# Optimization experiments

Hardware: AMD Instinct MI355X
Metric: run time of the kernel (lower is better)

Reference implementation:

```python
import jax, jax.numpy as jnp
import numpy as np

B, N, OBS, ACT, HID, GD, H = 1024, 64, 128, 16, 256, 64, 4
NEG_SLOPE = 0.2  # GAT leaky-relu alpha


def _gat(x, adj, W, a, concat):
    # x: (B,N,F), W: (H,F,D), a: (H,2D). Equivalent to concat([x_i,x_j]) . a
    # split as x_i.a1 + x_j.a2 -- same math, avoids the (B,H,N,N,2D) tensor.
    D = W.shape[-1]
    xt = jnp.einsum('bnf,hfd->bhnd', x, W)
    si = jnp.einsum('bhnd,hd->bhn', xt, a[:, :D])
    sj = jnp.einsum('bhnd,hd->bhn', xt, a[:, D:])
    s = jax.nn.leaky_relu(si[:, :, :, None] + sj[:, :, None, :], NEG_SLOPE)
    s = jnp.where(adj[:, None, :, :] == 0, -jnp.inf, s)
    w = jax.nn.softmax(s, axis=-1)
    out = jnp.einsum('bhij,bhjd->bhid', w, xt)
    if concat:
        b, n = x.shape[0], x.shape[1]
        return out.transpose(0, 2, 1, 3).reshape(b, n, -1)
    return out.mean(axis=1)


def _mlp3(x, w1, b1, w2, b2, w3, b3):
    # per-agent 3-layer MLP, weights stacked over agent axis n
    h = jax.nn.relu(jnp.einsum('bni,nih->bnh', x, w1) + b1)
    h = jax.nn.relu(jnp.einsum('bnh,nhk->bnk', h, w2) + b2)
    return jnp.einsum('bnk,nko->bno', h, w3) + b3


def _mlp2(x, w1, b1, w2, b2):
    h = jax.nn.relu(jnp.einsum('bni,nih->bnh', x, w1) + b1)
    return jnp.einsum('bnh,nho->bno', h, w2) + b2


def setup_inputs() -> dict:
    key = jax.random.key(0)
    ks = iter(jax.random.split(key, 64))

    def nrm(shape):
        fan_in = shape[-2] if len(shape) >= 2 else shape[-1]
        return jax.random.normal(next(ks), shape, jnp.float32) * np.float32(1.0 / np.sqrt(fan_in))

    AI = OBS + GD   # actor/critic input dim
    CI = OBS + ACT  # SCM / centralized per-agent input dim
    return dict(
        observations=jax.random.normal(next(ks), (B, N, OBS), jnp.float32),
        actions=jax.random.normal(next(ks), (B, N, ACT), jnp.float32),
        adj_matrix=jnp.ones((B, N, N), jnp.float32),
        causal_structure=jnp.eye(OBS, dtype=jnp.float32),
        gat_W=nrm((H, OBS, GD)), gat_a=nrm((H, 2 * GD)),
        cg_W0=nrm((H, OBS, GD)), cg_a0=nrm((H, 2 * GD)),
        cg_W1=nrm((H, H * GD, GD)), cg_a1=nrm((H, 2 * GD)),
        actor_w1=nrm((N, AI, HID)), actor_b1=jnp.zeros((N, HID), jnp.float32),
        actor_w2=nrm((N, HID, HID)), actor_b2=jnp.zeros((N, HID), jnp.float32),
        actor_w3=nrm((N, HID, ACT)), actor_b3=jnp.zeros((N, ACT), jnp.float32),
        critic_w1=nrm((N, AI, HID)), critic_b1=jnp.zeros((N, HID), jnp.float32),
        critic_w2=nrm((N, HID, HID)), critic_b2=jnp.zeros((N, HID), jnp.float32),
        critic_w3=nrm((N, HID, 1)), critic_b3=jnp.zeros((N, 1), jnp.float32),
        cent_w1=nrm((N * CI, HID)), cent_b1=jnp.zeros((HID,), jnp.float32),
        cent_w2=nrm((HID, HID)), cent_b2=jnp.zeros((HID,), jnp.float32),
        cent_w3=nrm((HID, N)), cent_b3=jnp.zeros((N,), jnp.float32),
        scm_causal=jnp.eye(N, dtype=jnp.float32),
        scm_mw1=nrm((N, CI, HID)), scm_mb1=jnp.zeros((N, HID), jnp.float32),
        scm_mw2=nrm((N, HID, HID)), scm_mb2=jnp.zeros((N, HID), jnp.float32),
        scm_mw3=nrm((N, HID, OBS)), scm_mb3=jnp.zeros((N, OBS), jnp.float32),
        scm_nw1=nrm((N, OBS, HID)), scm_nb1=jnp.zeros((N, HID), jnp.float32),
        scm_nw2=nrm((N, HID, OBS)), scm_nb2=jnp.zeros((N, OBS), jnp.float32),
    )


def reference(observations, actions, adj_matrix, causal_structure,
              gat_W, gat_a, cg_W0, cg_a0, cg_W1, cg_a1,
              actor_w1, actor_b1, actor_w2, actor_b2, actor_w3, actor_b3,
              critic_w1, critic_b1, critic_w2, critic_b2, critic_w3, critic_b3,
              cent_w1, cent_b1, cent_w2, cent_b2, cent_w3, cent_b3,
              scm_causal, scm_mw1, scm_mb1, scm_mw2, scm_mb2, scm_mw3, scm_mb3,
              scm_nw1, scm_nb1, scm_nw2, scm_nb2):
    # plain GAT communication features (concat=False -> head mean)
    gat_feat = _gat(observations, adj_matrix, gat_W, gat_a, False)
    # CausalGAT: causal mask on input features, then 2 GAT layers w/ ELU between
    xm = observations @ jax.nn.softmax(causal_structure, axis=-1)
    hcg = jax.nn.elu(_gat(xm, adj_matrix, cg_W0, cg_a0, True))
    causal_feat = _gat(hcg, adj_matrix, cg_W1, cg_a1, False)
    comm = gat_feat + causal_feat
    ai = jnp.concatenate([observations, comm], axis=-1)  # (B,N,OBS+GD)
    actor_out = _mlp3(ai, actor_w1, actor_b1, actor_w2, actor_b2, actor_w3, actor_b3)
    critic_out = _mlp3(ai, critic_w1, critic_b1, critic_w2, critic_b2, critic_w3, critic_b3)
    # centralized critic over flattened (obs, action) of all agents
    flat = jnp.concatenate([observations, actions], axis=-1).reshape(observations.shape[0], -1)
    hc = jax.nn.relu(flat @ cent_w1 + cent_b1)
    hc = jax.nn.relu(hc @ cent_w2 + cent_b2)
    cent_out = hc @ cent_w3 + cent_b3
    # SCM: per-agent causal mechanisms mixed by softmaxed causal matrix + noise model
    cw = jax.nn.softmax(scm_causal, axis=-1)
    combined = jnp.concatenate([observations, actions], axis=-1)
    ce = _mlp3(combined, scm_mw1, scm_mb1, scm_mw2, scm_mb2, scm_mw3, scm_mb3)
    se = jnp.einsum('ij,bjd->bid', cw, ce)
    noise = _mlp2(observations, scm_nw1, scm_nb1, scm_nw2, scm_nb2)
    scm_pred = se + noise
    return (actor_out, critic_out, cent_out, scm_pred)
```

## Files before the change

### kernel.cpp

```cpp
#include <hip/hip_runtime.h>
#include <hip/hip_bf16.h>
#include <math.h>

#define NB 1024
#define NAG 64
#define OBS 128
#define ACTD 16
#define HID 256
#define GD 64
#define NH 4

typedef short bhalf8 __attribute__((ext_vector_type(8)));
typedef float f32x4 __attribute__((ext_vector_type(4)));

__device__ inline unsigned short f2bf_u(float f) {
  __hip_bfloat16 h = __float2bfloat16(f);
  return *(unsigned short*)&h;
}
__device__ inline float bfu2f(unsigned short u) {
  unsigned v = ((unsigned)u) << 16;
  return *(float*)&v;
}
__device__ inline unsigned pk2(float x, float y) {
  float2 f2; f2.x = x; f2.y = y;
  __hip_bfloat162 h = __float22bfloat162_rn(f2);
  return *(unsigned*)&h;
}
__device__ inline unsigned fbits(float x) { return *(unsigned*)&x; }
__device__ inline float bcast(unsigned u) { return *(float*)&u; }
__device__ inline unsigned pkhi(float x, float y) {
  return (fbits(x) >> 16) | (fbits(y) & 0xFFFF0000u);
}
__device__ inline float hif(float x) {
  return bcast(fbits(x) & 0xFFFF0000u);
}

__global__ __launch_bounds__(64) void softmax_rows_k(const float* __restrict__ in,
                                                     float* __restrict__ out, int n) {
  int row = blockIdx.x;
  int lane = threadIdx.x;
  const float* r = in + (size_t)row * n;
  float m = -INFINITY;
  for (int j = lane; j < n; j += 64) m = fmaxf(m, r[j]);
#pragma unroll
  for (int off = 32; off; off >>= 1) m = fmaxf(m, __shfl_xor(m, off));
  float s = 0.f;
  for (int j = lane; j < n; j += 64) s += expf(r[j] - m);
#pragma unroll
  for (int off = 32; off; off >>= 1) s += __shfl_xor(s, off);
  float inv = 1.f / s;
  for (int j = lane; j < n; j += 64) out[(size_t)row * n + j] = expf(r[j] - m) * inv;
}

__global__ void cwbf_k(const float* __restrict__ cwsm, unsigned short* __restrict__ cw1,
                       unsigned short* __restrict__ cw2) {
  int idx = blockIdx.x * 256 + threadIdx.x;
  if (idx >= 4096) return;
  float v = cwsm[idx];
  unsigned short hi = f2bf_u(v);
  cw1[idx] = hi;
  cw2[idx] = f2bf_u(v - bfu2f(hi));
}

__global__ __launch_bounds__(256) void transpose_cvt_k(const float* __restrict__ in,
                                                       unsigned short* __restrict__ out,
                                                       int K, int N) {
  __shared__ float t[32][33];
  int k0 = blockIdx.x * 32, n0 = blockIdx.y * 32, z = blockIdx.z;
  int tx = threadIdx.x, ty = threadIdx.y;
  const float* ib = in + (size_t)z * K * N;
  unsigned short* ob = out + (size_t)z * N * K;
#pragma unroll
  for (int i = 0; i < 4; ++i) {
    int k = k0 + ty + 8 * i, n = n0 + tx;
    if (k < K && n < N) t[ty + 8 * i][tx] = ib[(size_t)k * N + n];
  }
  __syncthreads();
#pragma unroll
  for (int i = 0; i < 4; ++i) {
    int n = n0 + ty + 8 * i, k = k0 + tx;
    if (n < N && k < K) ob[(size_t)n * K + k] = f2bf_u(t[tx][ty + 8 * i]);
  }
}

__global__ void repack_wT_k(const float* __restrict__ W, unsigned short* __restrict__ WcT, int F) {
  int idx = blockIdx.x * 256 + threadIdx.x;
  if (idx >= NH * F * 64) return;
  int d = idx & 63;
  int f = (idx >> 6) % F;
  int h = idx / (F * 64);
  WcT[((size_t)(h * 64 + d)) * F + f] = f2bf_u(W[idx]);
}

__global__ __launch_bounds__(256) void gemm_mfma_k(
    const float* __restrict__ A, const unsigned short* __restrict__ BT,
    const float* __restrict__ bias, float* __restrict__ C,
    int M, int N, int K,
    long long lda, long long ldc,
    long long aBS, long long btBS, long long biasBS, long long cBS,
    int act, int kPerSplit) {
  __shared__ unsigned short As[2][64 * 40];
  __shared__ unsigned short Bs[2][64 * 40];
  int tid = threadIdx.x;
  int wave = tid >> 6, lane = tid & 63;
  int m0 = blockIdx.x * 64, n0 = blockIdx.y * 64;
  int z = blockIdx.z;
  const float* Ab;
  const unsigned short* Bb;
  const float* biasb = nullptr;
  float* Cb;
  int k_begin, k_end;
  if (kPerSplit > 0) {
    Ab = A; Bb = BT; Cb = C + (long long)z * cBS;
    k_begin = z * kPerSplit;
    k_end = k_begin + kPerSplit;
    if (k_end > K) k_end = K;
  } else {
    Ab = A + (long long)z * aBS;
    Bb = BT + (long long)z * btBS;
    if (bias) biasb = bias + (long long)z * biasBS;
    Cb = C + (long long)z * cBS;
    k_begin = 0; k_end = K;
  }
  int sr = tid >> 2;
  int sk = (tid & 3) * 8;
  int fr = lane & 15;
  int kq = (lane >> 4) * 8;

  f32x4 zf = {0.f, 0.f, 0.f, 0.f};
  f32x4 acc[4] = {zf, zf, zf, zf};

  const unsigned short* bRow = Bb + (long long)(n0 + sr) * K;
  bool bValid = (n0 + sr) < N;
  const float* aRow = Ab + (long long)(m0 + sr) * lda;

  int nt = (k_end - k_begin + 31) / 32;

  float av[8];
  uint4 bv;

  auto LOADT = [&](int t) {
    int kk = k_begin + 32 * t + sk;
    if (kk + 7 < k_end) {
      const float* ap = aRow + kk;
      *(float4*)&av[0] = *(const float4*)ap;
      *(float4*)&av[4] = *(const float4*)(ap + 4);
    } else {
#pragma unroll
      for (int j = 0; j < 8; ++j) av[j] = (kk + j < k_end) ? aRow[kk + j] : 0.f;
    }
    bv.x = bv.y = bv.z = bv.w = 0u;
    if (bValid) {
      if (kk + 7 < k_end) {
        bv = *(const uint4*)(bRow + kk);
      } else {
        unsigned short tb[8];
#pragma unroll
        for (int j = 0; j < 8; ++j) tb[j] = (kk + j < k_end) ? bRow[kk + j] : (unsigned short)0;
        bv.x = (unsigned)tb[0] | ((unsigned)tb[1] << 16);
        bv.y = (unsigned)tb[2] | ((unsigned)tb[3] << 16);
        bv.z = (unsigned)tb[4] | ((unsigned)tb[5] << 16);
        bv.w = (unsigned)tb[6] | ((unsigned)tb[7] << 16);
      }
    }
  };
  auto STORE = [&](int buf) {
    uint4 aw;
    aw.x = pk2(av[0], av[1]); aw.y = pk2(av[2], av[3]);
    aw.z = pk2(av[4], av[5]); aw.w = pk2(av[6], av[7]);
    *(uint4*)&As[buf][sr * 40 + sk] = aw;
    *(uint4*)&Bs[buf][sr * 40 + sk] = bv;
  };

  LOADT(0);
  STORE(0);
  if (nt > 1) LOADT(1);
  __syncthreads();

  for (int t = 0; t < nt; ++t) {
    int cur = t & 1;
    if (t + 1 < nt) {
      STORE(cur ^ 1);
      if (t + 2 < nt) LOADT(t + 2);
    }
    bhalf8 af = *(bhalf8*)&As[cur][(16 * wave + fr) * 40 + kq];
#pragma unroll
    for (int t4 = 0; t4 < 4; ++t4) {
      bhalf8 bf = *(bhalf8*)&Bs[cur][(16 * t4 + fr) * 40 + kq];
      acc[t4] = __builtin_amdgcn_mfma_f32_16x16x32_bf16(af, bf, acc[t4], 0, 0, 0);
    }
    if (t + 1 < nt) __syncthreads();
  }
  int rb = (lane >> 4) * 4;
#pragma unroll
  for (int t = 0; t < 4; ++t) {
    int col = n0 + 16 * t + fr;
    if (col < N) {
      float bv2 = biasb ? biasb[col] : 0.f;
#pragma unroll
      for (int r = 0; r < 4; ++r) {
        long long row = m0 + 16 * wave + rb + r;
        float v = acc[t][r] + bv2;
        if (act == 1) v = fmaxf(v, 0.f);
        Cb[row * ldc + col] = v;
      }
    }
  }
}

__global__ __launch_bounds__(256, 4) void gemm_mfma128_k(
    const float* __restrict__ A, const unsigned short* __restrict__ BT,
    const float* __restrict__ bias, float* __restrict__ C,
    int M, int N, int K,
    long long lda, long long ldc,
    long long aBS, long long btBS, long long biasBS, long long cBS,
    int act, int kPerSplit) {
  __shared__ unsigned short As[2][128 * 40];
  __shared__ unsigned short Bs[2][128 * 40];
  int tid = threadIdx.x;
  int wave = tid >> 6, lane = tid & 63;
  int m0 = blockIdx.x * 128, n0 = blockIdx.y * 128;
  int z = blockIdx.z;
  const float* Ab;
  const unsigned short* Bb;
  const float* biasb = nullptr;
  float* Cb;
  int k_begin, k_end;
  if (kPerSplit > 0) {
    Ab = A; Bb = BT; Cb = C + (long long)z * cBS;
    k_begin = z * kPerSplit;
    k_end = k_begin + kPerSplit;
    if (k_end > K) k_end = K;
  } else {
    Ab = A + (long long)z * aBS;
    Bb = BT + (long long)z * btBS;
    if (bias) biasb = bias + (long long)z * biasBS;
    Cb = C + (long long)z * cBS;
    k_begin = 0; k_end = K;
  }
  int sr = tid >> 1;
  int sk = (tid & 1) * 16;
  int mq = (wave >> 1) * 64;
  int nq = (wave & 1) * 64;
  int fr = lane & 15;
  int kq = (lane >> 4) * 8;

  f32x4 zf = {0.f, 0.f, 0.f, 0.f};
  f32x4 acc[4][4];
#pragma unroll
  for (int i = 0; i < 4; ++i)
#pragma unroll
    for (int j = 0; j < 4; ++j) acc[i][j] = zf;

  const float* aRow = Ab + (long long)(m0 + sr) * lda;
  const unsigned short* bRow = Bb + (long long)(n0 + sr) * K;
  bool bValid = (n0 + sr) < N;

  int nt = (k_end - k_begin + 31) / 32;

  float av[16];
  uint4 bv0, bv1;

  auto LOADT = [&](int t) {
    int kk = k_begin + 32 * t + sk;
    if (kk + 15 < k_end) {
      const float* ap = aRow + kk;
      *(float4*)&av[0]  = *(const float4*)ap;
      *(float4*)&av[4]  = *(const float4*)(ap + 4);
      *(float4*)&av[8]  = *(const float4*)(ap + 8);
      *(float4*)&av[12] = *(const float4*)(ap + 12);
    } else {
#pragma unroll
      for (int j = 0; j < 16; ++j) av[j] = (kk + j < k_end) ? aRow[kk + j] : 0.f;
    }
    bv0.x = bv0.y = bv0.z = bv0.w = 0u;
    bv1.x = bv1.y = bv1.z = bv1.w = 0u;
    if (bValid) {
      if (kk + 15 < k_end) {
        bv0 = *(const uint4*)(bRow + kk);
        bv1 = *(const uint4*)(bRow + kk + 8);
      } else {
        unsigned short tb[16];
#pragma unroll
        for (int j = 0; j < 16; ++j) tb[j] = (kk + j < k_end) ? bRow[kk + j] : (unsigned short)0;
        bv0.x = (unsigned)tb[0] | ((unsigned)tb[1] << 16);
        bv0.y = (unsigned)tb[2] | ((unsigned)tb[3] << 16);
        bv0.z = (unsigned)tb[4] | ((unsigned)tb[5] << 16);
        bv0.w = (unsigned)tb[6] | ((unsigned)tb[7] << 16);
        bv1.x = (unsigned)tb[8] | ((unsigned)tb[9] << 16);
        bv1.y = (unsigned)tb[10] | ((unsigned)tb[11] << 16);
        bv1.z = (unsigned)tb[12] | ((unsigned)tb[13] << 16);
        bv1.w = (unsigned)tb[14] | ((unsigned)tb[15] << 16);
      }
    }
  };
  auto STORE = [&](int buf) {
    uint4 aw0, aw1;
    aw0.x = pk2(av[0], av[1]);   aw0.y = pk2(av[2], av[3]);
    aw0.z = pk2(av[4], av[5]);   aw0.w = pk2(av[6], av[7]);
    aw1.x = pk2(av[8], av[9]);   aw1.y = pk2(av[10], av[11]);
    aw1.z = pk2(av[12], av[13]); aw1.w = pk2(av[14], av[15]);
    *(uint4*)&As[buf][sr * 40 + sk] = aw0;
    *(uint4*)&As[buf][sr * 40 + sk + 8] = aw1;
    *(uint4*)&Bs[buf][sr * 40 + sk] = bv0;
    *(uint4*)&Bs[buf][sr * 40 + sk + 8] = bv1;
  };

  LOADT(0);
  STORE(0);
  if (nt > 1) LOADT(1);
  __syncthreads();

  for (int t = 0; t < nt; ++t) {
    int cur = t & 1;
    if (t + 1 < nt) {
      STORE(cur ^ 1);
      if (t + 2 < nt) LOADT(t + 2);
    }
    bhalf8 af[4], bf[4];
#pragma unroll
    for (int i = 0; i < 4; ++i) af[i] = *(bhalf8*)&As[cur][(mq + 16 * i + fr) * 40 + kq];
#pragma unroll
    for (int j = 0; j < 4; ++j) bf[j] = *(bhalf8*)&Bs[cur][(nq + 16 * j + fr) * 40 + kq];
#pragma unroll
    for (int i = 0; i < 4; ++i)
#pragma unroll
      for (int j = 0; j < 4; ++j)
        acc[i][j] = __builtin_amdgcn_mfma_f32_16x16x32_bf16(af[i], bf[j], acc[i][j], 0, 0, 0);
    if (t + 1 < nt) __syncthreads();
  }
  int rb = (lane >> 4) * 4;
#pragma unroll
  for (int j = 0; j < 4; ++j) {
    int col = n0 + nq + 16 * j + fr;
    if (col < N) {
      float bv2 = biasb ? biasb[col] : 0.f;
#pragma unroll
      for (int i = 0; i < 4; ++i) {
#pragma unroll
        for (int r = 0; r < 4; ++r) {
          long long row = m0 + mq + 16 * i + rb + r;
          float v = acc[i][j][r] + bv2;
          if (act == 1) v = fmaxf(v, 0.f);
          Cb[row * ldc + col] = v;
        }
      }
    }
  }
}

__global__ __launch_bounds__(256, 4) void gat_attn4_k(
    const float* __restrict__ xt, const float* __restrict__ a,
    const float* __restrict__ adj, float* __restrict__ out, int mode) {
  int b = blockIdx.x;
  int tid = threadIdx.x;
  int wave = tid >> 6, lane = tid & 63;
  __shared__ unsigned short xT1[64 * 72];
  __shared__ unsigned short xT2[64 * 72];
  __shared__ unsigned short P1[64 * 72];
  __shared__ unsigned short P2[64 * 72];
  __shared__ float si_s[64], sj_s[64];

  const float* adjb = adj + (size_t)b * 4096;
  float adjv[16];
#pragma unroll
  for (int r = 0; r < 16; ++r) adjv[r] = adjb[(size_t)(wave * 16 + r) * 64 + lane];

  int lrow = tid >> 2;
  int cg = tid & 3;
  int fr = lane & 15;
  int kq = (lane >> 4) * 8;
  int ibase = wave * 16;

  bhalf8 ones;
#pragma unroll
  for (int u = 0; u < 8; ++u) ones[u] = (short)0x3F80;

  f32x4 zf = {0.f, 0.f, 0.f, 0.f};
  f32x4 accm[4] = {zf, zf, zf, zf};

  for (int h = 0; h < 4; ++h) {
    const float* xcol = xt + ((size_t)(b * 64 + 16 * wave)) * 256 + h * 64 + lane;
    float v[16];
#pragma unroll
    for (int u = 0; u < 16; ++u) v[u] = xcol[(size_t)u * 256];

    const float* xrow = xt + ((size_t)(b * 64 + lrow)) * 256 + h * 64 + cg * 16;
    const float* ah = a + h * 128;
    float p1 = 0.f, p2 = 0.f;
#pragma unroll
    for (int q = 0; q < 4; ++q) {
      float4 rv = *(const float4*)(xrow + 4 * q);
      int c = cg * 16 + 4 * q;
      p1 += rv.x * ah[c] + rv.y * ah[c + 1] + rv.z * ah[c + 2] + rv.w * ah[c + 3];
      p2 += rv.x * ah[64 + c] + rv.y * ah[64 + c + 1] + rv.z * ah[64 + c + 2] + rv.w * ah[64 + c + 3];
    }
    p1 += __shfl_xor(p1, 1); p1 += __shfl_xor(p1, 2);
    p2 += __shfl_xor(p2, 1); p2 += __shfl_xor(p2, 2);
    if (cg == 0) { si_s[lrow] = p1; sj_s[lrow] = p2; }

    {
      float lo[16];
      uint4 h0, h1, l0, l1;
#pragma unroll
      for (int u = 0; u < 16; ++u) lo[u] = v[u] - hif(v[u]);
      h0.x = pkhi(v[0], v[1]);    h0.y = pkhi(v[2], v[3]);
      h0.z = pkhi(v[4], v[5]);    h0.w = pkhi(v[6], v[7]);
      h1.x = pkhi(v[8], v[9]);    h1.y = pkhi(v[10], v[11]);
      h1.z = pkhi(v[12], v[13]);  h1.w = pkhi(v[14], v[15]);
      l0.x = pkhi(lo[0], lo[1]);   l0.y = pkhi(lo[2], lo[3]);
      l0.z = pkhi(lo[4], lo[5]);   l0.w = pkhi(lo[6], lo[7]);
      l1.x = pkhi(lo[8], lo[9]);   l1.y = pkhi(lo[10], lo[11]);
      l1.z = pkhi(lo[12], lo[13]); l1.w = pkhi(lo[14], lo[15]);
      int base = lane * 72 + 16 * wave;
      *(uint4*)&xT1[base] = h0;
      *(uint4*)&xT1[base + 8] = h1;
      *(uint4*)&xT2[base] = l0;
      *(uint4*)&xT2[base + 8] = l1;
    }
    __syncthreads();

    float sjv = sj_s[lane];
    float maxsj = sjv;
#pragma unroll
    for (int off = 32; off; off >>= 1) maxsj = fmaxf(maxsj, __shfl_xor(maxsj, off));
#pragma unroll
    for (int r = 0; r < 16; ++r) {
      int i = ibase + r;
      float siv = si_s[i];
      float tM = siv + maxsj;
      float Mi = tM > 0.f ? tM : 0.2f * tM;
      float e = siv + sjv;
      e = e > 0.f ? e : 0.2f * e;
      float p = (adjv[r] == 0.f) ? 0.f : __expf(e - Mi);
      unsigned up = fbits(p);
      float phf = bcast(up & 0xFFFF0000u);
      P1[i * 72 + lane] = (unsigned short)(up >> 16);
      float plo = p - phf;
      P2[i * 72 + lane] = (unsigned short)(fbits(plo) >> 16);
    }

    bhalf8 a1[2], a2[2];
#pragma unroll
    for (int ks = 0; ks < 2; ++ks) {
      a1[ks] = *(bhalf8*)&P1[(ibase + fr) * 72 + ks * 32 + kq];
      a2[ks] = *(bhalf8*)&P2[(ibase + fr) * 72 + ks * 32 + kq];
    }
    f32x4 accS = zf;
#pragma unroll
    for (int ks = 0; ks < 2; ++ks) {
      accS = __builtin_amdgcn_mfma_f32_16x16x32_bf16(a1[ks], ones, accS, 0, 0, 0);
      accS = __builtin_amdgcn_mfma_f32_16x16x32_bf16(a2[ks], ones, accS, 0, 0, 0);
    }
    f32x4 acc[4] = {zf, zf, zf, zf};
#pragma unroll
    for (int ks = 0; ks < 2; ++ks) {
#pragma unroll
      for (int t = 0; t < 4; ++t) {
        bhalf8 b1 = *(bhalf8*)&xT1[(16 * t + fr) * 72 + ks * 32 + kq];
        bhalf8 b2 = *(bhalf8*)&xT2[(16 * t + fr) * 72 + ks * 32 + kq];
        acc[t] = __builtin_amdgcn_mfma_f32_16x16x32_bf16(a1[ks], b1, acc[t], 0, 0, 0);
        acc[t] = __builtin_amdgcn_mfma_f32_16x16x32_bf16(a1[ks], b2, acc[t], 0, 0, 0);
        acc[t] = __builtin_amdgcn_mfma_f32_16x16x32_bf16(a2[ks], b1, acc[t], 0, 0, 0);
      }
    }
    f32x4 inv;
#pragma unroll
    for (int r = 0; r < 4; ++r) inv[r] = (accS[r] > 0.f) ? 1.f / accS[r] : 0.f;

    int rb = (lane >> 4) * 4;
    if (mode == 2) {
#pragma unroll
      for (int t = 0; t < 4; ++t) {
#pragma unroll
        for (int r = 0; r < 4; ++r) {
          int i = ibase + rb + r;
          float vv = acc[t][r] * inv[r];
          vv = vv > 0.f ? vv : __expf(vv) - 1.f;
          out[((size_t)(b * 64 + i)) * 256 + h * 64 + 16 * t + fr] = vv;
        }
      }
    } else {
#pragma unroll
      for (int t = 0; t < 4; ++t)
#pragma unroll
        for (int r = 0; r < 4; ++r) accm[t][r] += 0.25f * acc[t][r] * inv[r];
    }
    __syncthreads();
  }

  if (mode != 2) {
    int rb = (lane >> 4) * 4;
    float* cb = out + (size_t)b * 4096;
#pragma unroll
    for (int t = 0; t < 4; ++t) {
#pragma unroll
      for (int r = 0; r < 4; ++r) {
        int i = ibase + rb + r;
        int col = 16 * t + fr;
        if (mode == 1) cb[i * 64 + col] += accm[t][r];
        else cb[i * 64 + col] = accm[t][r];
      }
    }
  }
}

__global__ void build_ai_k(const float* __restrict__ obs, const float* __restrict__ comm,
                           float* __restrict__ ai) {
  size_t idx = (size_t)blockIdx.x * 256 + threadIdx.x;
  if (idx >= (size_t)NB * NAG * 192) return;
  int c = (int)(idx % 192);
  size_t bn = idx / 192;
  ai[idx] = (c < 128) ? obs[bn * 128 + c] : comm[bn * 64 + (c - 128)];
}

__global__ void build_combined_k(const float* __restrict__ obs, const float* __restrict__ act,
                                 float* __restrict__ cmb) {
  size_t idx = (size_t)blockIdx.x * 256 + threadIdx.x;
  if (idx >= (size_t)NB * NAG * 144) return;
  int c = (int)(idx % 144);
  size_t bn = idx / 144;
  cmb[idx] = (c < 128) ? obs[bn * 128 + c] : act[bn * 16 + (c - 128)];
}

__global__ void reduce_bias_relu_k(const float* __restrict__ part, const float* __restrict__ bias,
                                   float* __restrict__ out) {
  int idx = blockIdx.x * 256 + threadIdx.x;
  float s = 0.f;
#pragma unroll
  for (int zz = 0; zz < 16; ++zz) s += part[(size_t)zz * 262144 + idx];
  s += bias[idx & 255];
  out[idx] = fmaxf(s, 0.f);
}

__global__ __launch_bounds__(256, 4) void se_noise_mfma_k(
    const unsigned short* __restrict__ cw1, const unsigned short* __restrict__ cw2,
    const float* __restrict__ ce, const float* __restrict__ nz,
    float* __restrict__ out) {
  int b = blockIdx.x;
  int tid = threadIdx.x;
  int wave = tid >> 6, lane = tid & 63;
  __shared__ unsigned short xT1[128 * 72];
  __shared__ unsigned short xT2[128 * 72];

  int dd = tid & 127;
  int jh = tid >> 7;
  const float* cecol = ce + (size_t)b * 8192 + dd;
#pragma unroll
  for (int c = 0; c < 2; ++c) {
    int j0 = jh * 32 + c * 16;
    float v[16], lo[16];
#pragma unroll
    for (int u = 0; u < 16; ++u) v[u] = cecol[(size_t)(j0 + u) * 128];
#pragma unroll
    for (int u = 0; u < 16; ++u) lo[u] = v[u] - hif(v[u]);
    uint4 h0, h1, l0, l1;
    h0.x = pkhi(v[0], v[1]);    h0.y = pkhi(v[2], v[3]);
    h0.z = pkhi(v[4], v[5]);    h0.w = pkhi(v[6], v[7]);
    h1.x = pkhi(v[8], v[9]);    h1.y = pkhi(v[10], v[11]);
    h1.z = pkhi(v[12], v[13]);  h1.w = pkhi(v[14], v[15]);
    l0.x = pkhi(lo[0], lo[1]);   l0.y = pkhi(lo[2], lo[3]);
    l0.z = pkhi(lo[4], lo[5]);   l0.w = pkhi(lo[6], lo[7]);
    l1.x = pkhi(lo[8], lo[9]);   l1.y = pkhi(lo[10], lo[11]);
    l1.z = pkhi(lo[12], lo[13]); l1.w = pkhi(lo[14], lo[15]);
    int base = dd * 72 + j0;
    *(uint4*)&xT1[base] = h0;
    *(uint4*)&xT1[base + 8] = h1;
    *(uint4*)&xT2[base] = l0;
    *(uint4*)&xT2[base + 8] = l1;
  }
  __syncthreads();

  int fr = lane & 15;
  int kq = (lane >> 4) * 8;
  int dq = wave * 32;

  bhalf8 bb1[2][2], bb2[2][2];
#pragma unroll
  for (int dt = 0; dt < 2; ++dt)
#pragma unroll
    for (int ks = 0; ks < 2; ++ks) {
      bb1[dt][ks] = *(bhalf8*)&xT1[(dq + dt * 16 + fr) * 72 + ks * 32 + kq];
      bb2[dt][ks] = *(bhalf8*)&xT2[(dq + dt * 16 + fr) * 72 + ks * 32 + kq];
    }

  f32x4 zf = {0.f, 0.f, 0.f, 0.f};
  f32x4 acc[4][2];
#pragma unroll
  for (int it = 0; it < 4; ++it)
#pragma unroll
    for (int dt = 0; dt < 2; ++dt) acc[it][dt] = zf;

#pragma unroll
  for (int it = 0; it < 4; ++it) {
    bhalf8 a1[2], a2[2];
#pragma unroll
    for (int ks = 0; ks < 2; ++ks) {
      a1[ks] = *(const bhalf8*)(cw1 + (it * 16 + fr) * 64 + ks * 32 + kq);
      a2[ks] = *(const bhalf8*)(cw2 + (it * 16 + fr) * 64 + ks * 32 + kq);
    }
#pragma unroll
    for (int dt = 0; dt < 2; ++dt)
#pragma unroll
      for (int ks = 0; ks < 2; ++ks) {
        acc[it][dt] = __builtin_amdgcn_mfma_f32_16x16x32_bf16(a1[ks], bb1[dt][ks], acc[it][dt], 0, 0, 0);
        acc[it][dt] = __builtin_amdgcn_mfma_f32_16x16x32_bf16(a1[ks], bb2[dt][ks], acc[it][dt], 0, 0, 0);
        acc[it][dt] = __builtin_amdgcn_mfma_f32_16x16x32_bf16(a2[ks], bb1[dt][ks], acc[it][dt], 0, 0, 0);
      }
  }

  int rb = (lane >> 4) * 4;
#pragma unroll
  for (int it = 0; it < 4; ++it)
#pragma unroll
    for (int dt = 0; dt < 2; ++dt) {
      int dcol = dq + dt * 16 + fr;
#pragma unroll
      for (int r = 0; r < 4; ++r) {
        int i = it * 16 + rb + r;
        size_t off = (size_t)b * 8192 + (size_t)i * 128 + dcol;
        out[off] = acc[it][dt][r] + nz[off];
      }
    }
}

extern "C" void kernel_launch(void* const* d_in, const int* in_sizes, int n_in,
                              void* d_out, int out_size, void* d_ws, size_t ws_size,
                              hipStream_t stream) {
  (void)in_sizes; (void)n_in; (void)out_size; (void)ws_size;
  const float* obs = (const float*)d_in[0];
  const float* acts = (const float*)d_in[1];
  const float* adj = (const float*)d_in[2];
  const float* causal = (const float*)d_in[3];
  const float* gat_W = (const float*)d_in[4];
  const float* gat_a = (const float*)d_in[5];
  const float* cg_W0 = (const float*)d_in[6];
  const float* cg_a0 = (const float*)d_in[7];
  const float* cg_W1 = (const float*)d_in[8];
  const float* cg_a1 = (const float*)d_in[9];
  const float* aw1 = (const float*)d_in[10]; const float* ab1 = (const float*)d_in[11];
  const float* aw2 = (const float*)d_in[12]; const float* ab2 = (const float*)d_in[13];
  const float* aw3 = (const float*)d_in[14]; const float* ab3 = (const float*)d_in[15];
  const float* crw1 = (const float*)d_in[16]; const float* crb1 = (const float*)d_in[17];
  const float* crw2 = (const float*)d_in[18]; const float* crb2 = (const float*)d_in[19];
  const float* crw3 = (const float*)d_in[20]; const float* crb3 = (const float*)d_in[21];
  const float* cew1 = (const float*)d_in[22]; const float* ceb1 = (const float*)d_in[23];
  const float* cew2 = (const float*)d_in[24]; const float* ceb2 = (const float*)d_in[25];
  const float* cew3 = (const float*)d_in[26]; const float* ceb3 = (const float*)d_in[27];
  const float* scm_causal = (const float*)d_in[28];
  const float* mw1 = (const float*)d_in[29]; const float* mb1 = (const float*)d_in[30];
  const float* mw2 = (const float*)d_in[31]; const float* mb2 = (const float*)d_in[32];
  const float* mw3 = (const float*)d_in[33]; const float* mb3 = (const float*)d_in[34];
  const float* nw1 = (const float*)d_in[35]; const float* nb1 = (const float*)d_in[36];
  const float* nw2 = (const float*)d_in[37]; const float* nb2 = (const float*)d_in[38];

  float* ws = (float*)d_ws;
  float* Ssm  = ws;
  float* cwsm = ws + 16384;
  float* comm = ws + 20480;
  float* AI   = ws + 4214784;
  float* H1   = ws + 16797696;
  float* HCG  = ws + 33574912;
  unsigned short* wbf = (unsigned short*)(ws + 50352128);
  unsigned short* SsmT  = wbf;
  unsigned short* wcT   = wbf + 16384;
  unsigned short* aw1T  = wbf + 81920;
  unsigned short* aw2T  = wbf + 3227648;
  unsigned short* aw3T  = wbf + 7421952;
  unsigned short* crw1T = wbf + 7684096;
  unsigned short* crw2T = wbf + 10829824;
  unsigned short* crw3T = wbf + 15024128;
  unsigned short* cew1T = wbf + 15040512;
  unsigned short* cew2T = wbf + 17399808;
  unsigned short* cew3T = wbf + 17465344;
  unsigned short* mw1T  = wbf + 17481728;
  unsigned short* mw2T  = wbf + 19841024;
  unsigned short* mw3T  = wbf + 24035328;
  unsigned short* nw1T  = wbf + 26132480;
  unsigned short* nw2T  = wbf + 28229632;
  unsigned short* cw1g = (unsigned short*)ws;
  unsigned short* cw2g = cw1g + 4096;

  float* out_actor = (float*)d_out;
  float* out_critic = out_actor + 1048576;
  float* out_cent = out_critic + 65536;
  float* out_scm = out_cent + 65536;

  auto GEMM64 = [&](const float* A, const unsigned short* BT, const float* bias, float* C,
                    int M, int N, int K, long long lda, long long ldc,
                    long long aBS, long long btBS, long long biasBS, long long cBS,
                    int act, int gz, int kPerSplit) {
    dim3 grid(M / 64, (N + 63) / 64, gz);
    hipLaunchKernelGGL(gemm_mfma_k, grid, dim3(256), 0, stream, A, BT, bias, C, M, N, K,
                       lda, ldc, aBS, btBS, biasBS, cBS, act, kPerSplit);
  };
  auto GEMM128 = [&](const float* A, const unsigned short* BT, const float* bias, float* C,
                     int M, int N, int K, long long lda, long long ldc,
                     long long aBS, long long btBS, long long biasBS, long long cBS,
                     int act, int gz, int kPerSplit) {
    dim3 grid(M / 128, (N + 127) / 128, gz);
    hipLaunchKernelGGL(gemm_mfma128_k, grid, dim3(256), 0, stream, A, BT, bias, C, M, N, K,
                       lda, ldc, aBS, btBS, biasBS, cBS, act, kPerSplit);
  };
  auto TRN = [&](const float* in, unsigned short* out, int Z, int K, int N) {
    dim3 grid((K + 31) / 32, (N + 31) / 32, Z);
    hipLaunchKernelGGL(transpose_cvt_k, grid, dim3(32, 8), 0, stream, in, out, K, N);
  };

  hipLaunchKernelGGL(softmax_rows_k, dim3(128), dim3(64), 0, stream, causal, Ssm, 128);
  hipLaunchKernelGGL(softmax_rows_k, dim3(64), dim3(64), 0, stream, scm_causal, cwsm, 64);
  TRN(Ssm, SsmT, 1, 128, 128);
  hipLaunchKernelGGL(cwbf_k, dim3(16), dim3(256), 0, stream, cwsm, cw1g, cw2g);
  TRN(aw1, aw1T, 64, 192, 256);  TRN(aw2, aw2T, 64, 256, 256);  TRN(aw3, aw3T, 64, 256, 16);
  TRN(crw1, crw1T, 64, 192, 256); TRN(crw2, crw2T, 64, 256, 256); TRN(crw3, crw3T, 64, 256, 1);
  TRN(cew1, cew1T, 1, 9216, 256); TRN(cew2, cew2T, 1, 256, 256);  TRN(cew3, cew3T, 1, 256, 64);
  TRN(mw1, mw1T, 64, 144, 256);  TRN(mw2, mw2T, 64, 256, 256);  TRN(mw3, mw3T, 64, 256, 128);
  TRN(nw1, nw1T, 64, 128, 256);  TRN(nw2, nw2T, 64, 256, 128);

  hipLaunchKernelGGL(repack_wT_k, dim3((NH * 128 * 64 + 255) / 256), dim3(256), 0, stream, gat_W, wcT, 128);
  GEMM128(obs, wcT, nullptr, H1, 65536, 256, 128, 128, 256, 0, 0, 0, 0, 0, 1, 0);
  hipLaunchKernelGGL(gat_attn4_k, dim3(1024), dim3(256), 0, stream, H1, gat_a, adj, comm, 0);

  GEMM128(obs, SsmT, nullptr, HCG, 65536, 128, 128, 128, 128, 0, 0, 0, 0, 0, 1, 0);
  hipLaunchKernelGGL(repack_wT_k, dim3((NH * 128 * 64 + 255) / 256), dim3(256), 0, stream, cg_W0, wcT, 128);
  GEMM128(HCG, wcT, nullptr, H1, 65536, 256, 128, 128, 256, 0, 0, 0, 0, 0, 1, 0);
  hipLaunchKernelGGL(gat_attn4_k, dim3(1024), dim3(256), 0, stream, H1, cg_a0, adj, HCG, 2);
  hipLaunchKernelGGL(repack_wT_k, dim3((NH * 256 * 64 + 255) / 256), dim3(256), 0, stream, cg_W1, wcT, 256);
  GEMM128(HCG, wcT, nullptr, H1, 65536, 256, 256, 256, 256, 0, 0, 0, 0, 0, 1, 0);
  hipLaunchKernelGGL(gat_attn4_k, dim3(1024), dim3(256), 0, stream, H1, cg_a1, adj, comm, 1);

  hipLaunchKernelGGL(build_ai_k, dim3((12582912 + 255) / 256), dim3(256), 0, stream, obs, comm, AI);

  GEMM128(AI, aw1T, ab1, H1, 1024, 256, 192, 12288, 16384, 192, 49152, 256, 256, 1, 64, 0);
  GEMM128(H1, aw2T, ab2, HCG, 1024, 256, 256, 16384, 16384, 256, 65536, 256, 256, 1, 64, 0);
  GEMM64(HCG, aw3T, ab3, out_actor, 1024, 16, 256, 16384, 1024, 256, 4096, 16, 16, 0, 64, 0);

  GEMM128(AI, crw1T, crb1, H1, 1024, 256, 192, 12288, 16384, 192, 49152, 256, 256, 1, 64, 0);
  GEMM128(H1, crw2T, crb2, HCG, 1024, 256, 256, 16384, 16384, 256, 65536, 256, 256, 1, 64, 0);
  GEMM64(HCG, crw3T, crb3, out_critic, 1024, 1, 256, 16384, 64, 256, 256, 1, 1, 0, 64, 0);

  hipLaunchKernelGGL(build_combined_k, dim3((9437184 + 255) / 256), dim3(256), 0, stream, obs, acts, AI);
  GEMM128(AI, cew1T, nullptr, H1, 1024, 256, 9216, 9216, 256, 0, 0, 0, 262144, 0, 16, 576);
  hipLaunchKernelGGL(reduce_bias_relu_k, dim3(1024), dim3(256), 0, stream, H1, ceb1, HCG);
  GEMM64(HCG, cew2T, ceb2, H1, 1024, 256, 256, 256, 256, 0, 0, 0, 0, 1, 1, 0);
  GEMM64(H1, cew3T, ceb3, out_cent, 1024, 64, 256, 256, 64, 0, 0, 0, 0, 0, 1, 0);

  GEMM128(AI, mw1T, mb1, H1, 1024, 256, 144, 9216, 16384, 144, 36864, 256, 256, 1, 64, 0);
  GEMM128(H1, mw2T, mb2, HCG, 1024, 256, 256, 16384, 16384, 256, 65536, 256, 256, 1, 64, 0);
  GEMM128(HCG, mw3T, mb3, AI, 1024, 128, 256, 16384, 8192, 256, 32768, 128, 128, 0, 64, 0);

  GEMM128(obs, nw1T, nb1, H1, 1024, 256, 128, 8192, 16384, 128, 32768, 256, 256, 1, 64, 0);
  GEMM128(H1, nw2T, nb2, HCG, 1024, 128, 256, 16384, 8192, 256, 32768, 128, 128, 0, 64, 0);

  hipLaunchKernelGGL(se_noise_mfma_k, dim3(1024), dim3(256), 0, stream, cw1g, cw2g, AI, HCG, out_scm);
}
```

Before: 929.2 us.

## Store intermediate activations in bf16 between GEMMs to halve memory traffic

```diff
diff --git a/kernel.cpp b/kernel.cpp
--- a/kernel.cpp
+++ b/kernel.cpp
@@ -93,33 +93,32 @@
 }
 
 __global__ __launch_bounds__(256) void gemm_mfma_k(
-    const float* __restrict__ A, const unsigned short* __restrict__ BT,
-    const float* __restrict__ bias, float* __restrict__ C,
+    const void* __restrict__ A, const unsigned short* __restrict__ BT,
+    const float* __restrict__ bias, void* __restrict__ C,
     int M, int N, int K,
     long long lda, long long ldc,
     long long aBS, long long btBS, long long biasBS, long long cBS,
-    int act, int kPerSplit) {
+    int act, int kPerSplit, int aBf, int cBf) {
   __shared__ unsigned short As[2][64 * 40];
   __shared__ unsigned short Bs[2][64 * 40];
   int tid = threadIdx.x;
   int wave = tid >> 6, lane = tid & 63;
   int m0 = blockIdx.x * 64, n0 = blockIdx.y * 64;
   int z = blockIdx.z;
-  const float* Ab;
+  long long aOff, cOff;
   const unsigned short* Bb;
   const float* biasb = nullptr;
-  float* Cb;
   int k_begin, k_end;
   if (kPerSplit > 0) {
-    Ab = A; Bb = BT; Cb = C + (long long)z * cBS;
+    aOff = 0; Bb = BT; cOff = (long long)z * cBS;
     k_begin = z * kPerSplit;
     k_end = k_begin + kPerSplit;
     if (k_end > K) k_end = K;
   } else {
-    Ab = A + (long long)z * aBS;
+    aOff = (long long)z * aBS;
     Bb = BT + (long long)z * btBS;
     if (bias) biasb = bias + (long long)z * biasBS;
-    Cb = C + (long long)z * cBS;
+    cOff = (long long)z * cBS;
     k_begin = 0; k_end = K;
   }
   int sr = tid >> 2;
@@ -132,22 +131,40 @@
 
   const unsigned short* bRow = Bb + (long long)(n0 + sr) * K;
   bool bValid = (n0 + sr) < N;
-  const float* aRow = Ab + (long long)(m0 + sr) * lda;
+  const float* aRowF = (const float*)A + aOff + (long long)(m0 + sr) * lda;
+  const unsigned short* aRowH = (const unsigned short*)A + aOff + (long long)(m0 + sr) * lda;
+  float* CbF = (float*)C + cOff;
+  unsigned short* CbH = (unsigned short*)C + cOff;
 
   int nt = (k_end - k_begin + 31) / 32;
 
   float av[8];
+  uint4 awh;
   uint4 bv;
 
   auto LOADT = [&](int t) {
     int kk = k_begin + 32 * t + sk;
-    if (kk + 7 < k_end) {
-      const float* ap = aRow + kk;
-      *(float4*)&av[0] = *(const float4*)ap;
-      *(float4*)&av[4] = *(const float4*)(ap + 4);
+    if (aBf) {
+      if (kk + 7 < k_end) {
+        awh = *(const uint4*)(aRowH + kk);
+      } else {
+        unsigned short ta[8];
+#pragma unroll
+        for (int j = 0; j < 8; ++j) ta[j] = (kk + j < k_end) ? aRowH[kk + j] : (unsigned short)0;
+        awh.x = (unsigned)ta[0] | ((unsigned)ta[1] << 16);
+        awh.y = (unsigned)ta[2] | ((unsigned)ta[3] << 16);
+        awh.z = (unsigned)ta[4] | ((unsigned)ta[5] << 16);
+        awh.w = (unsigned)ta[6] | ((unsigned)ta[7] << 16);
+      }
     } else {
-#pragma unroll
-      for (int j = 0; j < 8; ++j) av[j] = (kk + j < k_end) ? aRow[kk + j] : 0.f;
+      if (kk + 7 < k_end) {
+        const float* ap = aRowF + kk;
+        *(float4*)&av[0] = *(const float4*)ap;
+        *(float4*)&av[4] = *(const float4*)(ap + 4);
+      } else {
+#pragma unroll
+        for (int j = 0; j < 8; ++j) av[j] = (kk + j < k_end) ? aRowF[kk + j] : 0.f;
+      }
     }
     bv.x = bv.y = bv.z = bv.w = 0u;
     if (bValid) {
@@ -166,8 +183,12 @@
   };
   auto STORE = [&](int buf) {
     uint4 aw;
-    aw.x = pk2(av[0], av[1]); aw.y = pk2(av[2], av[3]);
-    aw.z = pk2(av[4], av[5]); aw.w = pk2(av[6], av[7]);
+    if (aBf) {
+      aw = awh;
+    } else {
+      aw.x = pk2(av[0], av[1]); aw.y = pk2(av[2], av[3]);
+      aw.z = pk2(av[4], av[5]); aw.w = pk2(av[6], av[7]);
+    }
     *(uint4*)&As[buf][sr * 40 + sk] = aw;
     *(uint4*)&Bs[buf][sr * 40 + sk] = bv;
   };
@@ -202,40 +223,40 @@
         long long row = m0 + 16 * wave + rb + r;
         float v = acc[t][r] + bv2;
         if (act == 1) v = fmaxf(v, 0.f);
-        Cb[row * ldc + col] = v;
+        if (cBf) CbH[row * ldc + col] = f2bf_u(v);
+        else CbF[row * ldc + col] = v;
       }
     }
   }
 }
 
 __global__ __launch_bounds__(256, 4) void gemm_mfma128_k(
-    const float* __restrict__ A, const unsigned short* __restrict__ BT,
-    const float* __restrict__ bias, float* __restrict__ C,
+    const void* __restrict__ A, const unsigned short* __restrict__ BT,
+    const float* __restrict__ bias, void* __restrict__ C,
     int M, int N, int K,
     long long lda, long long ldc,
     long long aBS, long long btBS, long long biasBS, long long cBS,
-    int act, int kPerSplit) {
+    int act, int kPerSplit, int aBf, int cBf) {
   __shared__ unsigned short As[2][128 * 40];
   __shared__ unsigned short Bs[2][128 * 40];
   int tid = threadIdx.x;
   int wave = tid >> 6, lane = tid & 63;
   int m0 = blockIdx.x * 128, n0 = blockIdx.y * 128;
   int z = blockIdx.z;
-  const float* Ab;
+  long long aOff, cOff;
   const unsigned short* Bb;
   const float* biasb = nullptr;
-  float* Cb;
   int k_begin, k_end;
   if (kPerSplit > 0) {
-    Ab = A; Bb = BT; Cb = C + (long long)z * cBS;
+    aOff = 0; Bb = BT; cOff = (long long)z * cBS;
     k_begin = z * kPerSplit;
     k_end = k_begin + kPerSplit;
     if (k_end > K) k_end = K;
   } else {
-    Ab = A + (long long)z * aBS;
+    aOff = (long long)z * aBS;
     Bb = BT + (long long)z * btBS;
     if (bias) biasb = bias + (long long)z * biasBS;
-    Cb = C + (long long)z * cBS;
+    cOff = (long long)z * cBS;
     k_begin = 0; k_end = K;
   }
   int sr = tid >> 1;
@@ -252,26 +273,49 @@
 #pragma unroll
     for (int j = 0; j < 4; ++j) acc[i][j] = zf;
 
-  const float* aRow = Ab + (long long)(m0 + sr) * lda;
+  const float* aRowF = (const float*)A + aOff + (long long)(m0 + sr) * lda;
+  const unsigned short* aRowH = (const unsigned short*)A + aOff + (long long)(m0 + sr) * lda;
   const unsigned short* bRow = Bb + (long long)(n0 + sr) * K;
   bool bValid = (n0 + sr) < N;
+  float* CbF = (float*)C + cOff;
+  unsigned short* CbH = (unsigned short*)C + cOff;
 
   int nt = (k_end - k_begin + 31) / 32;
 
   float av[16];
+  uint4 awh0, awh1;
   uint4 bv0, bv1;
 
   auto LOADT = [&](int t) {
     int kk = k_begin + 32 * t + sk;
-    if (kk + 15 < k_end) {
-      const float* ap = aRow + kk;
-      *(float4*)&av[0]  = *(const float4*)ap;
-      *(float4*)&av[4]  = *(const float4*)(ap + 4);
-      *(float4*)&av[8]  = *(const float4*)(ap + 8);
-      *(float4*)&av[12] = *(const float4*)(ap + 12);
+    if (aBf) {
+      if (kk + 15 < k_end) {
+        awh0 = *(const uint4*)(aRowH + kk);
+        awh1 = *(const uint4*)(aRowH + kk + 8);
+      } else {
+        unsigned short ta[16];
+#pragma unroll
+        for (int j = 0; j < 16; ++j) ta[j] = (kk + j < k_end) ? aRowH[kk + j] : (unsigned short)0;
+        awh0.x = (unsigned)ta[0] | ((unsigned)ta[1] << 16);
+        awh0.y = (unsigned)ta[2] | ((unsigned)ta[3] << 16);
+        awh0.z = (unsigned)ta[4] | ((unsigned)ta[5] << 16);
+        awh0.w = (unsigned)ta[6] | ((unsigned)ta[7] << 16);
+        awh1.x = (unsigned)ta[8] | ((unsigned)ta[9] << 16);
+        awh1.y = (unsigned)ta[10] | ((unsigned)ta[11] << 16);
+        awh1.z = (unsigned)ta[12] | ((unsigned)ta[13] << 16);
+        awh1.w = (unsigned)ta[14] | ((unsigned)ta[15] << 16);
+      }
     } else {
-#pragma unroll
-      for (int j = 0; j < 16; ++j) av[j] = (kk + j < k_end) ? aRow[kk + j] : 0.f;
+      if (kk + 15 < k_end) {
+        const float* ap = aRowF + kk;
+        *(float4*)&av[0]  = *(const float4*)ap;
+        *(float4*)&av[4]  = *(const float4*)(ap + 4);
+        *(float4*)&av[8]  = *(const float4*)(ap + 8);
+        *(float4*)&av[12] = *(const float4*)(ap + 12);
+      } else {
+#pragma unroll
+        for (int j = 0; j < 16; ++j) av[j] = (kk + j < k_end) ? aRowF[kk + j] : 0.f;
+      }
     }
     bv0.x = bv0.y = bv0.z = bv0.w = 0u;
     bv1.x = bv1.y = bv1.z = bv1.w = 0u;
@@ -296,10 +340,14 @@
   };
   auto STORE = [&](int buf) {
     uint4 aw0, aw1;
-    aw0.x = pk2(av[0], av[1]);   aw0.y = pk2(av[2], av[3]);
-    aw0.z = pk2(av[4], av[5]);   aw0.w = pk2(av[6], av[7]);
-    aw1.x = pk2(av[8], av[9]);   aw1.y = pk2(av[10], av[11]);
-    aw1.z = pk2(av[12], av[13]); aw1.w = pk2(av[14], av[15]);
+    if (aBf) {
+      aw0 = awh0; aw1 = awh1;
+    } else {
+      aw0.x = pk2(av[0], av[1]);   aw0.y = pk2(av[2], av[3]);
+      aw0.z = pk2(av[4], av[5]);   aw0.w = pk2(av[6], av[7]);
+      aw1.x = pk2(av[8], av[9]);   aw1.y = pk2(av[10], av[11]);
+      aw1.z = pk2(av[12], av[13]); aw1.w = pk2(av[14], av[15]);
+    }
     *(uint4*)&As[buf][sr * 40 + sk] = aw0;
     *(uint4*)&As[buf][sr * 40 + sk + 8] = aw1;
     *(uint4*)&Bs[buf][sr * 40 + sk] = bv0;
@@ -342,7 +390,8 @@
           long long row = m0 + mq + 16 * i + rb + r;
           float v = acc[i][j][r] + bv2;
           if (act == 1) v = fmaxf(v, 0.f);
-          Cb[row * ldc + col] = v;
+          if (cBf) CbH[row * ldc + col] = f2bf_u(v);
+          else CbF[row * ldc + col] = v;
         }
       }
     }
@@ -470,6 +519,7 @@
 
     int rb = (lane >> 4) * 4;
     if (mode == 2) {
+      unsigned short* outh = (unsigned short*)out;
 #pragma unroll
       for (int t = 0; t < 4; ++t) {
 #pragma unroll
@@ -477,7 +527,7 @@
           int i = ibase + rb + r;
           float vv = acc[t][r] * inv[r];
           vv = vv > 0.f ? vv : __expf(vv) - 1.f;
-          out[((size_t)(b * 64 + i)) * 256 + h * 64 + 16 * t + fr] = vv;
+          outh[((size_t)(b * 64 + i)) * 256 + h * 64 + 16 * t + fr] = f2bf_u(vv);
         }
       }
     } else {
@@ -506,31 +556,33 @@
 }
 
 __global__ void build_ai_k(const float* __restrict__ obs, const float* __restrict__ comm,
-                           float* __restrict__ ai) {
+                           unsigned short* __restrict__ ai) {
   size_t idx = (size_t)blockIdx.x * 256 + threadIdx.x;
   if (idx >= (size_t)NB * NAG * 192) return;
   int c = (int)(idx % 192);
   size_t bn = idx / 192;
-  ai[idx] = (c < 128) ? obs[bn * 128 + c] : comm[bn * 64 + (c - 128)];
+  float v = (c < 128) ? obs[bn * 128 + c] : comm[bn * 64 + (c - 128)];
+  ai[idx] = f2bf_u(v);
 }
 
 __global__ void build_combined_k(const float* __restrict__ obs, const float* __restrict__ act,
-                                 float* __restrict__ cmb) {
+                                 unsigned short* __restrict__ cmb) {
   size_t idx = (size_t)blockIdx.x * 256 + threadIdx.x;
   if (idx >= (size_t)NB * NAG * 144) return;
   int c = (int)(idx % 144);
   size_t bn = idx / 144;
-  cmb[idx] = (c < 128) ? obs[bn * 128 + c] : act[bn * 16 + (c - 128)];
+  float v = (c < 128) ? obs[bn * 128 + c] : act[bn * 16 + (c - 128)];
+  cmb[idx] = f2bf_u(v);
 }
 
 __global__ void reduce_bias_relu_k(const float* __restrict__ part, const float* __restrict__ bias,
-                                   float* __restrict__ out) {
+                                   unsigned short* __restrict__ out) {
   int idx = blockIdx.x * 256 + threadIdx.x;
   float s = 0.f;
 #pragma unroll
   for (int zz = 0; zz < 16; ++zz) s += part[(size_t)zz * 262144 + idx];
   s += bias[idx & 255];
-  out[idx] = fmaxf(s, 0.f);
+  out[idx] = f2bf_u(fmaxf(s, 0.f));
 }
 
 __global__ __launch_bounds__(256, 4) void se_noise_mfma_k(
@@ -680,27 +732,30 @@
   unsigned short* nw2T  = wbf + 28229632;
   unsigned short* cw1g = (unsigned short*)ws;
   unsigned short* cw2g = cw1g + 4096;
+  unsigned short* AIb  = (unsigned short*)AI;
+  unsigned short* H1b  = (unsigned short*)H1;
+  unsigned short* HCGb = (unsigned short*)HCG;
 
   float* out_actor = (float*)d_out;
   float* out_critic = out_actor + 1048576;
   float* out_cent = out_critic + 65536;
   float* out_scm = out_cent + 65536;
 
-  auto GEMM64 = [&](const float* A, const unsigned short* BT, const float* bias, float* C,
+  auto GEMM64 = [&](const void* A, const unsigned short* BT, const float* bias, void* C,
                     int M, int N, int K, long long lda, long long ldc,
                     long long aBS, long long btBS, long long biasBS, long long cBS,
-                    int act, int gz, int kPerSplit) {
+                    int act, int gz, int kPerSplit, int aBf, int cBf) {
     dim3 grid(M / 64, (N + 63) / 64, gz);
     hipLaunchKernelGGL(gemm_mfma_k, grid, dim3(256), 0, stream, A, BT, bias, C, M, N, K,
-                       lda, ldc, aBS, btBS, biasBS, cBS, act, kPerSplit);
+                       lda, ldc, aBS, btBS, biasBS, cBS, act, kPerSplit, aBf, cBf);
   };
-  auto GEMM128 = [&](const float* A, const unsigned short* BT, const float* bias, float* C,
+  auto GEMM128 = [&](const void* A, const unsigned short* BT, const float* bias, void* C,
                      int M, int N, int K, long long lda, long long ldc,
                      long long aBS, long long btBS, long long biasBS, long long cBS,
-                     int act, int gz, int kPerSplit) {
+                     int act, int gz, int kPerSplit, int aBf, int cBf) {
     dim3 grid(M / 128, (N + 127) / 128, gz);
     hipLaunchKernelGGL(gemm_mfma128_k, grid, dim3(256), 0, stream, A, BT, bias, C, M, N, K,
-                       lda, ldc, aBS, btBS, biasBS, cBS, act, kPerSplit);
+                       lda, ldc, aBS, btBS, biasBS, cBS, act, kPerSplit, aBf, cBf);
   };
   auto TRN = [&](const float* in, unsigned short* out, int Z, int K, int N) {
     dim3 grid((K + 31) / 32, (N + 31) / 32, Z);
@@ -718,39 +773,39 @@
   TRN(nw1, nw1T, 64, 128, 256);  TRN(nw2, nw2T, 64, 256, 128);
 
   hipLaunchKernelGGL(repack_wT_k, dim3((NH * 128 * 64 + 255) / 256), dim3(256), 0, stream, gat_W, wcT, 128);
-  GEMM128(obs, wcT, nullptr, H1, 65536, 256, 128, 128, 256, 0, 0, 0, 0, 0, 1, 0);
+  GEMM128(obs, wcT, nullptr, H1, 65536, 256, 128, 128, 256, 0, 0, 0, 0, 0, 1, 0, 0, 0);
   hipLaunchKernelGGL(gat_attn4_k, dim3(1024), dim3(256), 0, stream, H1, gat_a, adj, comm, 0);
 
-  GEMM128(obs, SsmT, nullptr, HCG, 65536, 128, 128, 128, 128, 0, 0, 0, 0, 0, 1, 0);
+  GEMM128(obs, SsmT, nullptr, HCG, 65536, 128, 128, 128, 128, 0, 0, 0, 0, 0, 1, 0, 0, 1);
   hipLaunchKernelGGL(repack_wT_k, dim3((NH * 128 * 64 + 255) / 256), dim3(256), 0, stream, cg_W0, wcT, 128);
-  GEMM128(HCG, wcT, nullptr, H1, 65536, 256, 128, 128, 256, 0, 0, 0, 0, 0, 1, 0);
+  GEMM128(HCGb, wcT, nullptr, H1, 65536, 256, 128, 128, 256, 0, 0, 0, 0, 0, 1, 0, 1, 0);
   hipLaunchKernelGGL(gat_attn4_k, dim3(1024), dim3(256), 0, stream, H1, cg_a0, adj, HCG, 2);
   hipLaunchKernelGGL(repack_wT_k, dim3((NH * 256 * 64 + 255) / 256), dim3(256), 0, stream, cg_W1, wcT, 256);
-  GEMM128(HCG, wcT, nullptr, H1, 65536, 256, 256, 256, 256, 0, 0, 0, 0, 0, 1, 0);
+  GEMM128(HCGb, wcT, nullptr, H1, 65536, 256, 256, 256, 256, 0, 0, 0, 0, 0, 1, 0, 1, 0);
   hipLaunchKernelGGL(gat_attn4_k, dim3(1024), dim3(256), 0, stream, H1, cg_a1, adj, comm, 1);
 
-  hipLaunchKernelGGL(build_ai_k, dim3((12582912 + 255) / 256), dim3(256), 0, stream, obs, comm, AI);
-
-  GEMM128(AI, aw1T, ab1, H1, 1024, 256, 192, 12288, 16384, 192, 49152, 256, 256, 1, 64, 0);
-  GEMM128(H1, aw2T, ab2, HCG, 1024, 256, 256, 16384, 16384, 256, 65536, 256, 256, 1, 64, 0);
-  GEMM64(HCG, aw3T, ab3, out_actor, 1024, 16, 256, 16384, 1024, 256, 4096, 16, 16, 0, 64, 0);
-
-  GEMM128(AI, crw1T, crb1, H1, 1024, 256, 192, 12288, 16384, 192, 49152, 256, 256, 1, 64, 0);
-  GEMM128(H1, crw2T, crb2, HCG, 1024, 256, 256, 16384, 16384, 256, 65536, 256, 256, 1, 64, 0);
-  GEMM64(HCG, crw3T, crb3, out_critic, 1024, 1, 256, 16384, 64, 256, 256, 1, 1, 0, 64, 0);
-
-  hipLaunchKernelGGL(build_combined_k, dim3((9437184 + 255) / 256), dim3(256), 0, stream, obs, acts, AI);
-  GEMM128(AI, cew1T, nullptr, H1, 1024, 256, 9216, 9216, 256, 0, 0, 0, 262144, 0, 16, 576);
-  hipLaunchKernelGGL(reduce_bias_relu_k, dim3(1024), dim3(256), 0, stream, H1, ceb1, HCG);
-  GEMM64(HCG, cew2T, ceb2, H1, 1024, 256, 256, 256, 256, 0, 0, 0, 0, 1, 1, 0);
-  GEMM64(H1, cew3T, ceb3, out_cent, 1024, 64, 256, 256, 64, 0, 0, 0, 0, 0, 1, 0);
-
-  GEMM128(AI, mw1T, mb1, H1, 1024, 256, 144, 9216, 16384, 144, 36864, 256, 256, 1, 64, 0);
-  GEMM128(H1, mw2T, mb2, HCG, 1024, 256, 256, 16384, 16384, 256, 65536, 256, 256, 1, 64, 0);
-  GEMM128(HCG, mw3T, mb3, AI, 1024, 128, 256, 16384, 8192, 256, 32768, 128, 128, 0, 64, 0);
-
-  GEMM128(obs, nw1T, nb1, H1, 1024, 256, 128, 8192, 16384, 128, 32768, 256, 256, 1, 64, 0);
-  GEMM128(H1, nw2T, nb2, HCG, 1024, 128, 256, 16384, 8192, 256, 32768, 128, 128, 0, 64, 0);
+  hipLaunchKernelGGL(build_ai_k, dim3((12582912 + 255) / 256), dim3(256), 0, stream, obs, comm, AIb);
+
+  GEMM128(AIb, aw1T, ab1, H1b, 1024, 256, 192, 12288, 16384, 192, 49152, 256, 256, 1, 64, 0, 1, 1);
+  GEMM128(H1b, aw2T, ab2, HCGb, 1024, 256, 256, 16384, 16384, 256, 65536, 256, 256, 1, 64, 0, 1, 1);
+  GEMM64(HCGb, aw3T, ab3, out_actor, 1024, 16, 256, 16384, 1024, 256, 4096, 16, 16, 0, 64, 0, 1, 0);
+
+  GEMM128(AIb, crw1T, crb1, H1b, 1024, 256, 192, 12288, 16384, 192, 49152, 256, 256, 1, 64, 0, 1, 1);
+  GEMM128(H1b, crw2T, crb2, HCGb, 1024, 256, 256, 16384, 16384, 256, 65536, 256, 256, 1, 64, 0, 1, 1);
+  GEMM64(HCGb, crw3T, crb3, out_critic, 1024, 1, 256, 16384, 64, 256, 256, 1, 1, 0, 64, 0, 1, 0);
+
+  hipLaunchKernelGGL(build_combined_k, dim3((9437184 + 255) / 256), dim3(256), 0, stream, obs, acts, AIb);
+  GEMM128(AIb, cew1T, nullptr, H1, 1024, 256, 9216, 9216, 256, 0, 0, 0, 262144, 0, 16, 576, 1, 0);
+  hipLaunchKernelGGL(reduce_bias_relu_k, dim3(1024), dim3(256), 0, stream, H1, ceb1, HCGb);
+  GEMM64(HCGb, cew2T, ceb2, H1b, 1024, 256, 256, 256, 256, 0, 0, 0, 0, 1, 1, 0, 1, 1);
+  GEMM64(H1b, cew3T, ceb3, out_cent, 1024, 64, 256, 256, 64, 0, 0, 0, 0, 0, 1, 0, 1, 0);
+
+  GEMM128(AIb, mw1T, mb1, H1b, 1024, 256, 144, 9216, 16384, 144, 36864, 256, 256, 1, 64, 0, 1, 1);
+  GEMM128(H1b, mw2T, mb2, HCGb, 1024, 256, 256, 16384, 16384, 256, 65536, 256, 256, 1, 64, 0, 1, 1);
+  GEMM128(HCGb, mw3T, mb3, AI, 1024, 128, 256, 16384, 8192, 256, 32768, 128, 128, 0, 64, 0, 1, 0);
+
+  GEMM128(obs, nw1T, nb1, H1b, 1024, 256, 128, 8192, 16384, 128, 32768, 256, 256, 1, 64, 0, 0, 1);
+  GEMM128(H1b, nw2T, nb2, HCG, 1024, 128, 256, 16384, 8192, 256, 32768, 128, 128, 0, 64, 0, 1, 0);
 
   hipLaunchKernelGGL(se_noise_mfma_k, dim3(1024), dim3(256), 0, stream, cw1g, cw2g, AI, HCG, out_scm);
 }
```

Result: faster. 906.4 us (-2.5%).
